# Kernel optimization log

Measured on AMD Instinct MI355X. Metric: run time of the kernel, lower is better.

## Reference

```python
import jax, jax.numpy as jnp
import numpy as np

EPS = 1e-06


def setup_inputs() -> dict:
    key = jax.random.key(0)
    k1, k2, k3 = jax.random.split(key, 3)
    B, L, S, C = 128, 512, 512, 64
    q = jax.random.normal(k1, (B, L, C), dtype=jnp.float32)
    k = jax.random.normal(k2, (B, S, C), dtype=jnp.float32)
    labels = jax.random.randint(k3, (B, L, S), 0, 2, dtype=jnp.int64)
    return {"q": q, "k": k, "labels": labels}


def reference(q, k, labels):
    # sim: [B, L, S], mapped to (0, 1) via (1 + cos-like sim) / 2
    sim = (1.0 + jnp.einsum('blc,bsc->bls', q, k)) * 0.5

    # column-wise stats (over L) -> [B, S]; torch.std uses ddof=1 (unbiased)
    col = (jnp.max(sim, axis=1) - jnp.mean(sim, axis=1)) / jnp.std(sim, axis=1, ddof=1)
    sharp1 = jax.nn.softmax(col, axis=-1)  # [B, S]

    # row-wise stats (over S) -> [B, L]
    row = (jnp.max(sim, axis=2) - jnp.mean(sim, axis=2)) / jnp.std(sim, axis=2, ddof=1)
    sharp2 = jax.nn.softmax(row, axis=-1)  # [B, L]

    simc = jnp.clip(sim, EPS, 1.0 - EPS)
    nll = -jnp.log(simc)                    # [B, L, S]
    nll_neg = -jnp.log(1.0 - simc)          # [B, L, S]

    pos = (labels == 1).astype(sim.dtype)
    neg = (labels == 0).astype(sim.dtype)

    # masked sums per sample, weighted by sharpness (broadcast over rows/cols)
    loss1 = jnp.sum(nll * sharp1[:, None, :] * pos, axis=(1, 2))  # [B]
    loss2 = jnp.sum(nll * sharp2[:, :, None] * pos, axis=(1, 2))  # [B]
    loss3 = jnp.sum(nll_neg * neg, axis=(1, 2)) / jnp.sum(neg, axis=(1, 2))  # [B]

    losses = (loss1 + loss2) * 0.5 + loss3
    return (sharp1, jnp.mean(losses))
```

## Files before the change

### kernel.cpp

```cpp
#include <hip/hip_runtime.h>

#define EPSF 1e-6f

constexpr int B = 128, L = 512, S = 512, C = 64;
constexpr int TILE_R = 128;
constexpr int TILES  = L / TILE_R;
constexpr int CHUNK  = 64;
constexpr int NCHUNK = S / CHUNK;
constexpr int QSTR   = 132;
constexpr int KSTR   = 68;

constexpr size_t WS_COLMAX = 0;
constexpr size_t WS_COLSUM = WS_COLMAX + (size_t)B * TILES * S;
constexpr size_t WS_COLSSQ = WS_COLSUM + (size_t)B * TILES * S;
constexpr size_t WS_COLP1  = WS_COLSSQ + (size_t)B * TILES * S;
constexpr size_t WS_ROWMAX = WS_COLP1  + (size_t)B * TILES * S;
constexpr size_t WS_ROWSUM = WS_ROWMAX + (size_t)B * L;
constexpr size_t WS_ROWSSQ = WS_ROWSUM + (size_t)B * L;
constexpr size_t WS_ROWP2  = WS_ROWSSQ + (size_t)B * L;
constexpr size_t WS_NEGS   = WS_ROWP2  + (size_t)B * L;
constexpr size_t WS_NEGC   = WS_NEGS   + (size_t)B * TILES;

__global__ __launch_bounds__(256, 2)
void pass1_kernel(const float* __restrict__ q, const float* __restrict__ kmat,
                  const int* __restrict__ labels, float* __restrict__ ws)
{
    __shared__ float qs[C][QSTR];
    __shared__ float ks[C][KSTR];
    __shared__ float colred[4][CHUNK][4];
    __shared__ float nred[4][2];

    const int bidx = blockIdx.x;
    const int b    = bidx / TILES;
    const int tile = bidx % TILES;
    const int tid  = threadIdx.x;
    const int tx   = tid & 15;
    const int ty   = tid >> 4;
    const int lane = tid & 63;
    const int wave = tid >> 6;
    const int rowbase = tile * TILE_R;
    const int r0 = ty * 8;
    const int c0 = tx * 4;

    float* colmax_p = ws + WS_COLMAX;
    float* colsum_p = ws + WS_COLSUM;
    float* colssq_p = ws + WS_COLSSQ;
    float* colp1_p  = ws + WS_COLP1;
    float* rowmax_p = ws + WS_ROWMAX;
    float* rowsum_p = ws + WS_ROWSUM;
    float* rowssq_p = ws + WS_ROWSSQ;
    float* rowp2_p  = ws + WS_ROWP2;
    float* negs_p   = ws + WS_NEGS;
    float* negc_p   = ws + WS_NEGC;

    const float* qb = q + ((size_t)b * L + rowbase) * C;
    for (int it = tid; it < TILE_R * C; it += 256) {
        qs[it & 63][it >> 6] = qb[it];
    }

    float rmax[8], rsum[8], rssq[8], rp2[8];
#pragma unroll
    for (int i = 0; i < 8; ++i) { rmax[i] = -3.4e38f; rsum[i] = 0.f; rssq[i] = 0.f; rp2[i] = 0.f; }
    float negsum = 0.f, negcnt = 0.f;

    const float* kb = kmat + (size_t)b * S * C;
    const int*   lb = labels + ((size_t)b * L + rowbase) * S;

    for (int ch = 0; ch < NCHUNK; ++ch) {
        __syncthreads();
        const float* kc = kb + (size_t)ch * CHUNK * C;
        for (int it = tid; it < CHUNK * C; it += 256) {
            ks[it & 63][it >> 6] = kc[it];
        }
        __syncthreads();

        float acc[8][4];
#pragma unroll
        for (int i = 0; i < 8; ++i)
#pragma unroll
            for (int j = 0; j < 4; ++j) acc[i][j] = 0.f;

#pragma unroll 4
        for (int kk = 0; kk < C; ++kk) {
            float4 a0 = *(const float4*)&qs[kk][r0];
            float4 a1 = *(const float4*)&qs[kk][r0 + 4];
            float4 bb = *(const float4*)&ks[kk][c0];
#pragma unroll
            for (int j = 0; j < 4; ++j) {
                float bj = (j == 0) ? bb.x : (j == 1) ? bb.y : (j == 2) ? bb.z : bb.w;
                acc[0][j] = fmaf(a0.x, bj, acc[0][j]);
                acc[1][j] = fmaf(a0.y, bj, acc[1][j]);
                acc[2][j] = fmaf(a0.z, bj, acc[2][j]);
                acc[3][j] = fmaf(a0.w, bj, acc[3][j]);
                acc[4][j] = fmaf(a1.x, bj, acc[4][j]);
                acc[5][j] = fmaf(a1.y, bj, acc[5][j]);
                acc[6][j] = fmaf(a1.z, bj, acc[6][j]);
                acc[7][j] = fmaf(a1.w, bj, acc[7][j]);
            }
        }

        float cmax[4], csum[4], cssq[4], cp1[4];
#pragma unroll
        for (int j = 0; j < 4; ++j) { cmax[j] = -3.4e38f; csum[j] = 0.f; cssq[j] = 0.f; cp1[j] = 0.f; }

#pragma unroll
        for (int i = 0; i < 8; ++i) {
            const int* lrow = lb + (size_t)(r0 + i) * S + ch * CHUNK + c0;
            int4 lv = *(const int4*)lrow;
            int labv[4] = {lv.x, lv.y, lv.z, lv.w};
#pragma unroll
            for (int j = 0; j < 4; ++j) {
                float sim = fmaf(0.5f, acc[i][j], 0.5f);
                rmax[i] = fmaxf(rmax[i], sim);
                rsum[i] += sim;
                rssq[i] = fmaf(sim, sim, rssq[i]);
                cmax[j] = fmaxf(cmax[j], sim);
                csum[j] += sim;
                cssq[j] = fmaf(sim, sim, cssq[j]);
                float sc  = fminf(fmaxf(sim, EPSF), 1.f - EPSF);
                bool  isp = (labv[j] == 1);
                float pos = isp ? 1.f : 0.f;
                float t   = isp ? sc : (1.f - sc);
                float nl  = -__logf(t);
                float pn  = pos * nl;
                rp2[i] += pn;
                cp1[j] += pn;
                negsum += nl - pn;
                negcnt += 1.f - pos;
            }
        }

#pragma unroll
        for (int j = 0; j < 4; ++j) {
#pragma unroll
            for (int m = 16; m <= 32; m <<= 1) {
                cmax[j] = fmaxf(cmax[j], __shfl_xor(cmax[j], m, 64));
                csum[j] += __shfl_xor(csum[j], m, 64);
                cssq[j] += __shfl_xor(cssq[j], m, 64);
                cp1[j]  += __shfl_xor(cp1[j],  m, 64);
            }
        }
        if (lane < 16) {
#pragma unroll
            for (int j = 0; j < 4; ++j) {
                colred[wave][lane * 4 + j][0] = cmax[j];
                colred[wave][lane * 4 + j][1] = csum[j];
                colred[wave][lane * 4 + j][2] = cssq[j];
                colred[wave][lane * 4 + j][3] = cp1[j];
            }
        }
        __syncthreads();
        if (tid < CHUNK) {
            float m0 = colred[0][tid][0], s1 = colred[0][tid][1];
            float s2 = colred[0][tid][2], pp = colred[0][tid][3];
#pragma unroll
            for (int w = 1; w < 4; ++w) {
                m0 = fmaxf(m0, colred[w][tid][0]);
                s1 += colred[w][tid][1];
                s2 += colred[w][tid][2];
                pp += colred[w][tid][3];
            }
            size_t idx = ((size_t)b * TILES + tile) * S + ch * CHUNK + tid;
            colmax_p[idx] = m0; colsum_p[idx] = s1; colssq_p[idx] = s2; colp1_p[idx] = pp;
        }
    }

#pragma unroll
    for (int i = 0; i < 8; ++i) {
#pragma unroll
        for (int m = 1; m <= 8; m <<= 1) {
            rmax[i] = fmaxf(rmax[i], __shfl_xor(rmax[i], m, 64));
            rsum[i] += __shfl_xor(rsum[i], m, 64);
            rssq[i] += __shfl_xor(rssq[i], m, 64);
            rp2[i]  += __shfl_xor(rp2[i],  m, 64);
        }
    }
    if (tx == 0) {
#pragma unroll
        for (int i = 0; i < 8; ++i) {
            size_t idx = (size_t)b * L + rowbase + r0 + i;
            rowmax_p[idx] = rmax[i]; rowsum_p[idx] = rsum[i];
            rowssq_p[idx] = rssq[i]; rowp2_p[idx]  = rp2[i];
        }
    }

#pragma unroll
    for (int m = 1; m <= 32; m <<= 1) {
        negsum += __shfl_xor(negsum, m, 64);
        negcnt += __shfl_xor(negcnt, m, 64);
    }
    if (lane == 0) { nred[wave][0] = negsum; nred[wave][1] = negcnt; }
    __syncthreads();
    if (tid == 0) {
        float ns = 0.f, nc = 0.f;
        for (int w = 0; w < 4; ++w) { ns += nred[w][0]; nc += nred[w][1]; }
        negs_p[bidx] = ns; negc_p[bidx] = nc;
    }
}

template <bool MAX>
__device__ inline float bred(float v, float* red)
{
#pragma unroll
    for (int m = 1; m <= 32; m <<= 1) {
        float o = __shfl_xor(v, m, 64);
        v = MAX ? fmaxf(v, o) : (v + o);
    }
    const int wave = threadIdx.x >> 6;
    const int lane = threadIdx.x & 63;
    if (lane == 0) red[wave] = v;
    __syncthreads();
    if (threadIdx.x == 0) {
        float r = red[0];
        for (int w = 1; w < 8; ++w) r = MAX ? fmaxf(r, red[w]) : (r + red[w]);
        red[8] = r;
    }
    __syncthreads();
    float out = red[8];
    __syncthreads();
    return out;
}

__global__ __launch_bounds__(512)
void pass2_kernel(const float* __restrict__ ws, float* __restrict__ out)
{
    __shared__ float red[9];
    const int b = blockIdx.x;
    const int s = threadIdx.x;

    if (blockIdx.y == 0) {
        const float* colmax_p = ws + WS_COLMAX;
        const float* colsum_p = ws + WS_COLSUM;
        const float* colssq_p = ws + WS_COLSSQ;
        const float* colp1_p  = ws + WS_COLP1;

        float m = -3.4e38f, sm = 0.f, sq = 0.f, p1 = 0.f;
#pragma unroll
        for (int t = 0; t < TILES; ++t) {
            size_t idx = ((size_t)b * TILES + t) * S + s;
            m = fmaxf(m, colmax_p[idx]);
            sm += colsum_p[idx];
            sq += colssq_p[idx];
            p1 += colp1_p[idx];
        }
        float mean  = sm * (1.f / L);
        float var   = (sq - sm * sm * (1.f / L)) * (1.f / (L - 1));
        float score = (m - mean) / sqrtf(var);

        float gmax = bred<true>(score, red);
        float e    = __expf(score - gmax);
        float esum = bred<false>(e, red);
        float sharp1 = e / esum;
        out[(size_t)b * S + s] = sharp1;
        float loss1 = bred<false>(sharp1 * p1, red);
        if (s == 0) atomicAdd(out + (size_t)B * S, loss1 * (0.5f / B));
    } else {
        const float* rowmax_p = ws + WS_ROWMAX;
        const float* rowsum_p = ws + WS_ROWSUM;
        const float* rowssq_p = ws + WS_ROWSSQ;
        const float* rowp2_p  = ws + WS_ROWP2;
        const float* negs_p   = ws + WS_NEGS;
        const float* negc_p   = ws + WS_NEGC;

        size_t ridx = (size_t)b * L + s;
        float m2 = rowmax_p[ridx], sm2 = rowsum_p[ridx];
        float sq2 = rowssq_p[ridx], p2 = rowp2_p[ridx];
        float mean2  = sm2 * (1.f / S);
        float var2   = (sq2 - sm2 * sm2 * (1.f / S)) * (1.f / (S - 1));
        float score2 = (m2 - mean2) / sqrtf(var2);

        float gmax2 = bred<true>(score2, red);
        float e2    = __expf(score2 - gmax2);
        float esum2 = bred<false>(e2, red);
        float loss2 = bred<false>((e2 / esum2) * p2, red);

        if (s == 0) {
            float ns = 0.f, nc = 0.f;
            for (int t = 0; t < TILES; ++t) { ns += negs_p[b * TILES + t]; nc += negc_p[b * TILES + t]; }
            atomicAdd(out + (size_t)B * S, (0.5f * loss2 + ns / nc) * (1.f / B));
        }
    }
}

extern "C" void kernel_launch(void* const* d_in, const int* in_sizes, int n_in,
                              void* d_out, int out_size, void* d_ws, size_t ws_size,
                              hipStream_t stream)
{
    const float* q      = (const float*)d_in[0];
    const float* k      = (const float*)d_in[1];
    const int*   labels = (const int*)d_in[2];
    float* out = (float*)d_out;
    float* ws  = (float*)d_ws;

    hipMemsetAsync((char*)d_out + (size_t)B * S * sizeof(float), 0, sizeof(float), stream);

    pass1_kernel<<<dim3(B * TILES), dim3(256), 0, stream>>>(q, k, labels, ws);
    pass2_kernel<<<dim3(B, 2), dim3(512), 0, stream>>>(ws, out);
}
```

Baseline: 286.0 us.

## Halve row tile to 64, use 4x4 microtile and vectorized transposed staging

Shrinks each block's row tile from 128 to 64 rows, so each thread computes a 4x4 sim microtile instead of 8x4. This doubles the block count and raises the launch-bounds occupancy hint from 2 to 4 blocks per SIMD-group. Q and K are now staged into LDS through a float4 load-and-transpose helper instead of scalar strided stores. The trade-off is twice as many per-tile column partials in the workspace and recomputation of the K chunk loads per block, with lower arithmetic intensity per LDS read.

```diff
diff --git a/kernel.cpp b/kernel.cpp
--- a/kernel.cpp
+++ b/kernel.cpp
@@ -3,12 +3,11 @@
 #define EPSF 1e-6f
 
 constexpr int B = 128, L = 512, S = 512, C = 64;
-constexpr int TILE_R = 128;
+constexpr int TILE_R = 64;
 constexpr int TILES  = L / TILE_R;
 constexpr int CHUNK  = 64;
 constexpr int NCHUNK = S / CHUNK;
-constexpr int QSTR   = 132;
-constexpr int KSTR   = 68;
+constexpr int STR    = 68;
 
 constexpr size_t WS_COLMAX = 0;
 constexpr size_t WS_COLSUM = WS_COLMAX + (size_t)B * TILES * S;
@@ -21,12 +20,26 @@
 constexpr size_t WS_NEGS   = WS_ROWP2  + (size_t)B * L;
 constexpr size_t WS_NEGC   = WS_NEGS   + (size_t)B * TILES;
 
-__global__ __launch_bounds__(256, 2)
+__device__ inline void stage_T(const float* __restrict__ g, float (*lds)[STR], int tid)
+{
+    const int r0 = (tid & 15) * 4;
+    const int c0 = (tid >> 4) * 4;
+    float4 r0v = *(const float4*)&g[(r0 + 0) * 64 + c0];
+    float4 r1v = *(const float4*)&g[(r0 + 1) * 64 + c0];
+    float4 r2v = *(const float4*)&g[(r0 + 2) * 64 + c0];
+    float4 r3v = *(const float4*)&g[(r0 + 3) * 64 + c0];
+    *(float4*)&lds[c0 + 0][r0] = make_float4(r0v.x, r1v.x, r2v.x, r3v.x);
+    *(float4*)&lds[c0 + 1][r0] = make_float4(r0v.y, r1v.y, r2v.y, r3v.y);
+    *(float4*)&lds[c0 + 2][r0] = make_float4(r0v.z, r1v.z, r2v.z, r3v.z);
+    *(float4*)&lds[c0 + 3][r0] = make_float4(r0v.w, r1v.w, r2v.w, r3v.w);
+}
+
+__global__ __launch_bounds__(256, 4)
 void pass1_kernel(const float* __restrict__ q, const float* __restrict__ kmat,
                   const int* __restrict__ labels, float* __restrict__ ws)
 {
-    __shared__ float qs[C][QSTR];
-    __shared__ float ks[C][KSTR];
+    __shared__ float qs[C][STR];
+    __shared__ float ks[C][STR];
     __shared__ float colred[4][CHUNK][4];
     __shared__ float nred[4][2];
 
@@ -39,7 +52,7 @@
     const int lane = tid & 63;
     const int wave = tid >> 6;
     const int rowbase = tile * TILE_R;
-    const int r0 = ty * 8;
+    const int r0 = ty * 4;
     const int c0 = tx * 4;
 
     float* colmax_p = ws + WS_COLMAX;
@@ -53,14 +66,11 @@
     float* negs_p   = ws + WS_NEGS;
     float* negc_p   = ws + WS_NEGC;
 
-    const float* qb = q + ((size_t)b * L + rowbase) * C;
-    for (int it = tid; it < TILE_R * C; it += 256) {
-        qs[it & 63][it >> 6] = qb[it];
-    }
-
-    float rmax[8], rsum[8], rssq[8], rp2[8];
-#pragma unroll
-    for (int i = 0; i < 8; ++i) { rmax[i] = -3.4e38f; rsum[i] = 0.f; rssq[i] = 0.f; rp2[i] = 0.f; }
+    stage_T(q + ((size_t)b * L + rowbase) * C, qs, tid);
+
+    float rmax[4], rsum[4], rssq[4], rp2[4];
+#pragma unroll
+    for (int i = 0; i < 4; ++i) { rmax[i] = -3.4e38f; rsum[i] = 0.f; rssq[i] = 0.f; rp2[i] = 0.f; }
     float negsum = 0.f, negcnt = 0.f;
 
     const float* kb = kmat + (size_t)b * S * C;
@@ -68,35 +78,26 @@
 
     for (int ch = 0; ch < NCHUNK; ++ch) {
         __syncthreads();
-        const float* kc = kb + (size_t)ch * CHUNK * C;
-        for (int it = tid; it < CHUNK * C; it += 256) {
-            ks[it & 63][it >> 6] = kc[it];
-        }
+        stage_T(kb + (size_t)ch * CHUNK * C, ks, tid);
         __syncthreads();
 
-        float acc[8][4];
-#pragma unroll
-        for (int i = 0; i < 8; ++i)
+        float acc[4][4];
+#pragma unroll
+        for (int i = 0; i < 4; ++i)
 #pragma unroll
             for (int j = 0; j < 4; ++j) acc[i][j] = 0.f;
 
 #pragma unroll 4
         for (int kk = 0; kk < C; ++kk) {
-            float4 a0 = *(const float4*)&qs[kk][r0];
-            float4 a1 = *(const float4*)&qs[kk][r0 + 4];
-            float4 bb = *(const float4*)&ks[kk][c0];
-#pragma unroll
-            for (int j = 0; j < 4; ++j) {
-                float bj = (j == 0) ? bb.x : (j == 1) ? bb.y : (j == 2) ? bb.z : bb.w;
-                acc[0][j] = fmaf(a0.x, bj, acc[0][j]);
-                acc[1][j] = fmaf(a0.y, bj, acc[1][j]);
-                acc[2][j] = fmaf(a0.z, bj, acc[2][j]);
-                acc[3][j] = fmaf(a0.w, bj, acc[3][j]);
-                acc[4][j] = fmaf(a1.x, bj, acc[4][j]);
-                acc[5][j] = fmaf(a1.y, bj, acc[5][j]);
-                acc[6][j] = fmaf(a1.z, bj, acc[6][j]);
-                acc[7][j] = fmaf(a1.w, bj, acc[7][j]);
-            }
+            float4 av = *(const float4*)&qs[kk][r0];
+            float4 bv = *(const float4*)&ks[kk][c0];
+            float a[4] = {av.x, av.y, av.z, av.w};
+            float bb[4] = {bv.x, bv.y, bv.z, bv.w};
+#pragma unroll
+            for (int i = 0; i < 4; ++i)
+#pragma unroll
+                for (int j = 0; j < 4; ++j)
+                    acc[i][j] = fmaf(a[i], bb[j], acc[i][j]);
         }
 
         float cmax[4], csum[4], cssq[4], cp1[4];
@@ -104,7 +105,7 @@
         for (int j = 0; j < 4; ++j) { cmax[j] = -3.4e38f; csum[j] = 0.f; cssq[j] = 0.f; cp1[j] = 0.f; }
 
 #pragma unroll
-        for (int i = 0; i < 8; ++i) {
+        for (int i = 0; i < 4; ++i) {
             const int* lrow = lb + (size_t)(r0 + i) * S + ch * CHUNK + c0;
             int4 lv = *(const int4*)lrow;
             int labv[4] = {lv.x, lv.y, lv.z, lv.w};
@@ -166,7 +167,7 @@
     }
 
 #pragma unroll
-    for (int i = 0; i < 8; ++i) {
+    for (int i = 0; i < 4; ++i) {
 #pragma unroll
         for (int m = 1; m <= 8; m <<= 1) {
             rmax[i] = fmaxf(rmax[i], __shfl_xor(rmax[i], m, 64));
@@ -177,7 +178,7 @@
     }
     if (tx == 0) {
 #pragma unroll
-        for (int i = 0; i < 8; ++i) {
+        for (int i = 0; i < 4; ++i) {
             size_t idx = (size_t)b * L + rowbase + r0 + i;
             rowmax_p[idx] = rmax[i]; rowsum_p[idx] = rsum[i];
             rowssq_p[idx] = rssq[i]; rowp2_p[idx]  = rp2[i];
```

New measurement: 282.1 us. Within noise of the previous version (-1.4%).
